# Kernel optimization log

Measured on AMD Instinct MI355X. Metric: run time of the kernel, lower is better.

Reference implementation:

```python
import jax, jax.numpy as jnp
import numpy as np

N_NODES = 20000
N_EDGES = 200000
C = 64             # channel multiplicity (hidden_irreps = 64x0e + 64x1o)
LMAX = 3
NLM = (LMAX + 1) ** 2   # 16 spherical-harmonic components
NUM_ELEM = 10
R_DIM = 8          # radial embedding out dim
MLP_H = 64
AVG_NEI = 10.0
L_OF_LM = np.repeat(np.arange(LMAX + 1), 2 * np.arange(LMAX + 1) + 1)  # [16] l index per lm slot


def setup_inputs() -> dict:
    key = jax.random.key(0)
    k = jax.random.split(key, 16)
    f32 = jnp.float32
    elems = jax.random.randint(k[0], (N_NODES,), 0, NUM_ELEM)
    one_hot = jax.nn.one_hot(elems, NUM_ELEM, dtype=f32)
    node_features = jax.random.normal(k[1], (N_NODES, C), dtype=f32)
    angular_embedding = jax.random.normal(k[2], (N_EDGES, NLM), dtype=f32)
    radial_embedding = jax.random.normal(k[3], (N_EDGES, R_DIM), dtype=f32)
    edge_index = jax.random.randint(k[4], (2, N_EDGES), 0, N_NODES)

    def w(kk, shape, fan_in):  # e3nn-style 1/sqrt(fan_in) normalization baked into init
        return jax.random.normal(kk, shape, dtype=f32) / float(np.sqrt(fan_in))

    W_up = w(k[5], (C, C), C)
    W_mlp1 = w(k[6], (R_DIM, MLP_H), R_DIM)
    W_mlp2 = w(k[7], (MLP_H, MLP_H), MLP_H)
    W_mlp3 = w(k[8], (MLP_H, MLP_H), MLP_H)
    W_mlp4 = w(k[9], (MLP_H, (LMAX + 1) * C), MLP_H)
    W_lin = w(k[10], (LMAX + 1, C, C), C)
    W_skip = w(k[11], (C, NUM_ELEM, C), C * NUM_ELEM)
    W_c0 = jax.random.normal(k[12], (NUM_ELEM, C), dtype=f32)
    W_c1 = jax.random.normal(k[13], (NUM_ELEM, C), dtype=f32)
    W_p0 = w(k[14], (C, C), C)
    W_p1 = w(k[15], (C, C), C)
    return dict(node_features=node_features, one_hot=one_hot,
                angular_embedding=angular_embedding, radial_embedding=radial_embedding,
                W_up=W_up, W_mlp1=W_mlp1, W_mlp2=W_mlp2, W_mlp3=W_mlp3, W_mlp4=W_mlp4,
                W_lin=W_lin, W_skip=W_skip, W_c0=W_c0, W_c1=W_c1, W_p0=W_p0, W_p1=W_p1,
                edge_index=edge_index)


def reference(node_features, one_hot, angular_embedding, radial_embedding,
              W_up, W_mlp1, W_mlp2, W_mlp3, W_mlp4, W_lin, W_skip,
              W_c0, W_c1, W_p0, W_p1, edge_index):
    sender, receiver = edge_index[0], edge_index[1]
    n = node_features.shape[0]
    # ---- interaction block (RealAgnosticResidual; node feats are pure scalars 64x0e) ----
    x = node_features @ W_up                                    # linear_up [N,C]
    h = jax.nn.silu(radial_embedding @ W_mlp1)                  # radial MLP -> per-edge TP weights
    h = jax.nn.silu(h @ W_mlp2)
    h = jax.nn.silu(h @ W_mlp3)
    tp_w = (h @ W_mlp4).reshape(-1, LMAX + 1, C)                # [E,4,C] (one weight per l path, uvu)
    w_lm = tp_w[:, L_OF_LM, :]                                  # [E,16,C]
    # uvu tensor product of 0e node feats with spherical harmonics (CG trivial for 0e x l -> l)
    msg = x[sender][:, None, :] * angular_embedding[:, :, None] * w_lm   # [E,16,C]
    agg = jax.ops.segment_sum(msg, receiver, num_segments=n) / AVG_NEI   # scatter-sum [N,16,C]
    feats = jnp.einsum('nmc,mck->nmk', agg, W_lin[L_OF_LM])     # per-l channel-mixing linear [N,16,C]
    # residual skip FCTP(64x0e, 10x0e -> hidden): only the 0e block is connected
    sc0 = jnp.einsum('nc,na,cak->nk', node_features, one_hot, W_skip)    # [N,C]
    # ---- equivariant product basis block (correlation = 1) ----
    wn0 = one_hot @ W_c0                                        # element-dependent weights [N,C]
    wn1 = one_hot @ W_c1
    f0 = feats[:, 0, :] * wn0                                   # l=0 output [N,C]
    f1 = feats[:, 1:4, :] * wn1[:, None, :]                     # l=1 output [N,3,C]
    out0 = f0 @ W_p0 + sc0                                      # [N,C]
    out1 = jnp.einsum('nmc,ck->nmk', f1, W_p1)                  # [N,3,C] (sc 1o block is zero)
    # flatten to e3nn channel-major irreps layout -> node_env [N, C*(1+3)]
    return jnp.concatenate([out0, jnp.swapaxes(out1, 1, 2).reshape(n, -1)], axis=-1)
```

## Files before the change

### kernel.cpp

```cpp
#include <hip/hip_runtime.h>

typedef __attribute__((ext_vector_type(8))) short s16x8;
typedef __attribute__((ext_vector_type(4))) float f32x4;

__device__ inline float bf2f(ushort u) {
    union { unsigned int i; float f; } v; v.i = ((unsigned)u) << 16; return v.f;
}
__device__ inline float u2f(unsigned u) {
    union { unsigned int i; float f; } v; v.i = u; return v.f;
}
__device__ inline ushort f2bf(float f) {
    union { float f; unsigned int i; } v; v.f = f;
    unsigned r = v.i + 0x7FFFu + ((v.i >> 16) & 1u);
    return (ushort)(r >> 16);
}
__device__ inline unsigned cvt_pk(float lo, float hi) {
    unsigned d;
    asm("v_cvt_pk_bf16_f32 %0, %1, %2" : "=v"(d) : "v"(lo), "v"(hi));
    return d;
}
__device__ inline float silu_f(float x) {
    float e;
    asm("v_exp_f32 %0, %1" : "=v"(e) : "v"(x * -1.44269504f));
    float d = 1.f + e, r;
    asm("v_rcp_f32 %0, %1" : "=v"(r) : "v"(d));
    return x * r;
}

__global__ __launch_bounds__(256) void prep_up_kernel(
    const float* __restrict__ nf, const float* __restrict__ W_up,
    ushort* __restrict__ x_ws,
    const float* __restrict__ W1, const float* __restrict__ W2,
    const float* __restrict__ W3, const float* __restrict__ W4,
    const float* __restrict__ W_lin, const float* __restrict__ Wp0,
    const float* __restrict__ Wp1, const float* __restrict__ W_skip,
    ushort* __restrict__ wimg, int* __restrict__ counts, int N) {
    __shared__ float sW[64 * 64];
    __shared__ float sNf[32][64];
    int tid = threadIdx.x;
    int nub = N / 32;
    if ((int)blockIdx.x < nub) {
        size_t n0 = (size_t)blockIdx.x * 32;
        for (int i = tid; i < 4096; i += 256) sW[i] = W_up[i];
        for (int i = tid; i < 2048; i += 256) {
            int r = i >> 6, c = i & 63;
            sNf[r][c] = nf[(n0 + r) * 64 + c];
        }
        __syncthreads();
        int r = tid >> 3, k0 = (tid & 7) * 8;
        float acc[8] = {0, 0, 0, 0, 0, 0, 0, 0};
        #pragma unroll 4
        for (int c = 0; c < 64; ++c) {
            float v = sNf[r][c];
            const float* wr = &sW[c * 64 + k0];
            #pragma unroll
            for (int j = 0; j < 8; ++j) acc[j] += v * wr[j];
        }
        uint4 val;
        val.x = cvt_pk(acc[0], acc[1]);
        val.y = cvt_pk(acc[2], acc[3]);
        val.z = cvt_pk(acc[4], acc[5]);
        val.w = cvt_pk(acc[6], acc[7]);
        *(uint4*)(x_ws + (n0 + r) * 64 + k0) = val;
        return;
    }
    int idx = ((int)blockIdx.x - nub) * 256 + tid;
    if (idx < N) counts[idx] = 0;
    if (idx < 4096) {
        int m = idx >> 6, k = idx & 63;
        int dst = m * 64 + ((((k >> 3) ^ (m & 7))) << 3) + (k & 7);
        wimg[dst] = (k < 8) ? f2bf(W1[k * 64 + m]) : (ushort)0;
    } else if (idx < 8192) {
        int i = idx - 4096;
        int m = i >> 6, k = i & 63;
        int dst = 4096 + m * 64 + ((((k >> 3) ^ (m & 7))) << 3) + (k & 7);
        wimg[dst] = f2bf(W2[k * 64 + m]);
    } else if (idx < 12288) {
        int i = idx - 8192;
        int m = i >> 6, k = i & 63;
        int dst = 8192 + m * 64 + ((((k >> 3) ^ (m & 7))) << 3) + (k & 7);
        wimg[dst] = f2bf(W3[k * 64 + m]);
    } else if (idx < 20480) {
        int i = idx - 12288;
        int m = i >> 6, k = i & 63;
        int dst = 12288 + m * 64 + ((((k >> 3) ^ (m & 7))) << 3) + (k & 7);
        wimg[dst] = f2bf(W4[k * 256 + m]);
    } else if (idx < 29696) {
        int i = idx - 20480;
        int row = i / 72, k = i % 72;
        int l = row >> 6, col = row & 63;
        wimg[idx] = (k < 64) ? f2bf(W_lin[l * 4096 + k * 64 + col]) : (ushort)0;
    } else if (idx < 38912) {
        int i = idx - 29696;
        int row = i / 72, k = i % 72;
        int l = row >> 6, col = row & 63;
        const float* Wp = l ? Wp1 : Wp0;
        wimg[idx] = (k < 64) ? f2bf(Wp[k * 64 + col]) : (ushort)0;
    } else if (idx < 79872) {
        int i = idx - 38912;
        wimg[idx] = f2bf(W_skip[i]);
    }
}

__global__ __launch_bounds__(256) void hist_kernel(const int* __restrict__ recv,
                                                   int* __restrict__ counts,
                                                   int* __restrict__ rank, int E) {
    int e = blockIdx.x * 256 + threadIdx.x;
    if (e < E) rank[e] = atomicAdd(&counts[recv[e]], 1);
}

__global__ __launch_bounds__(1024) void scan_kernel(const int* __restrict__ counts,
                                                    int* __restrict__ offsets, int n) {
    __shared__ int wsums[16];
    int tid = threadIdx.x, lane = tid & 63, wid = tid >> 6;
    int CH = (n + 1023) >> 10;
    int base = tid * CH;
    int cnt[20];
    int tot = 0;
    if (CH <= 20) {
        #pragma unroll
        for (int j = 0; j < 20; ++j) {
            int i = base + j;
            cnt[j] = (j < CH && i < n) ? counts[i] : 0;
            tot += cnt[j];
        }
    } else {
        for (int j = 0; j < CH; ++j) {
            int i = base + j;
            if (i < n) tot += counts[i];
        }
    }
    int v = tot;
    for (int off = 1; off < 64; off <<= 1) {
        int t = __shfl_up(v, off, 64);
        if (lane >= off) v += t;
    }
    if (lane == 63) wsums[wid] = v;
    __syncthreads();
    if (tid == 0) {
        int acc = 0;
        for (int w = 0; w < 16; ++w) { int t = wsums[w]; wsums[w] = acc; acc += t; }
    }
    __syncthreads();
    int excl = wsums[wid] + v - tot;
    if (CH <= 20) {
        #pragma unroll
        for (int j = 0; j < 20; ++j) {
            int i = base + j;
            if (j < CH && i < n) { offsets[i] = excl; excl += cnt[j]; }
        }
    } else {
        for (int j = 0; j < CH; ++j) {
            int i = base + j;
            if (i < n) { offsets[i] = excl; excl += counts[i]; }
        }
    }
    if (tid == 1023) offsets[n] = excl;
}

__global__ __launch_bounds__(256) void edge_mlp_kernel(
    const int* __restrict__ recv, const int* __restrict__ sender,
    const int* __restrict__ rank, const int* __restrict__ offsets,
    const float* __restrict__ radial, int2* __restrict__ csr_es,
    const ushort* __restrict__ wimg, unsigned* __restrict__ tpw32, int E) {
    __shared__ __align__(16) ushort sB[4][2048];
    int tid = threadIdx.x, lane = tid & 63, wave = tid >> 6;
    int n = lane & 15, hi = lane >> 4;
    int base = blockIdx.x * 128 + wave * 32;
    if (base >= E) return;
    int eA = base + n, eB = base + 16 + n;
    bool okA = eA < E, okB = eB < E;
    int eAc = min(eA, E - 1), eBc = min(eB, E - 1);

    char* bAq = (char*)sB[wave];
    char* bBq = (char*)sB[wave] + 2048;
    int n7 = n & 7;

    s16x8 bRA, bRB;
    #pragma unroll
    for (int j = 0; j < 8; ++j) { bRA[j] = 0; bRB[j] = 0; }
    if (hi == 0) {
        float4 a0 = *(const float4*)(radial + (size_t)eAc * 8);
        float4 a1 = *(const float4*)(radial + (size_t)eAc * 8 + 4);
        float4 c0 = *(const float4*)(radial + (size_t)eBc * 8);
        float4 c1 = *(const float4*)(radial + (size_t)eBc * 8 + 4);
        union { s16x8 v; uint4 u; } pa, pb;
        pa.u.x = cvt_pk(a0.x, a0.y); pa.u.y = cvt_pk(a0.z, a0.w);
        pa.u.z = cvt_pk(a1.x, a1.y); pa.u.w = cvt_pk(a1.z, a1.w);
        pb.u.x = cvt_pk(c0.x, c0.y); pb.u.y = cvt_pk(c0.z, c0.w);
        pb.u.z = cvt_pk(c1.x, c1.y); pb.u.w = cvt_pk(c1.z, c1.w);
        bRA = pa.v; bRB = pb.v;
        if (okA) {
            int2 es; es.x = eA; es.y = sender[eA];
            csr_es[offsets[recv[eA]] + rank[eA]] = es;
        }
        if (okB) {
            int2 es; es.x = eB; es.y = sender[eB];
            csr_es[offsets[recv[eB]] + rank[eB]] = es;
        }
    }

    f32x4 zero = {0.f, 0.f, 0.f, 0.f};
    f32x4 dA[4], dB[4];

    #pragma unroll
    for (int mt = 0; mt < 4; ++mt) {
        int row = mt * 16 + n, r7 = row & 7;
        s16x8 w = *(const s16x8*)(wimg + row * 64 + ((hi ^ r7) << 3));
        dA[mt] = __builtin_amdgcn_mfma_f32_16x16x32_bf16(w, bRA, zero, 0, 0, 0);
        dB[mt] = __builtin_amdgcn_mfma_f32_16x16x32_bf16(w, bRB, zero, 0, 0, 0);
    }
    #pragma unroll
    for (int mt = 0; mt < 4; ++mt) {
        int slot = mt * 2 + (hi >> 1);
        int off = ((slot ^ n7) << 4) + (hi & 1) * 8;
        uint2 vA = {cvt_pk(silu_f(dA[mt][0]), silu_f(dA[mt][1])),
                    cvt_pk(silu_f(dA[mt][2]), silu_f(dA[mt][3]))};
        *(uint2*)(bAq + n * 128 + off) = vA;
        uint2 vB = {cvt_pk(silu_f(dB[mt][0]), silu_f(dB[mt][1])),
                    cvt_pk(silu_f(dB[mt][2]), silu_f(dB[mt][3]))};
        *(uint2*)(bBq + n * 128 + off) = vB;
    }
    s16x8 b0A = *(const s16x8*)(bAq + n * 128 + ((hi ^ n7) << 4));
    s16x8 b1A = *(const s16x8*)(bAq + n * 128 + (((4 + hi) ^ n7) << 4));
    s16x8 b0B = *(const s16x8*)(bBq + n * 128 + ((hi ^ n7) << 4));
    s16x8 b1B = *(const s16x8*)(bBq + n * 128 + (((4 + hi) ^ n7) << 4));

    #pragma unroll
    for (int mt = 0; mt < 4; ++mt) {
        int row = mt * 16 + n, r7 = row & 7;
        s16x8 w0 = *(const s16x8*)(wimg + 4096 + row * 64 + ((hi ^ r7) << 3));
        s16x8 w1 = *(const s16x8*)(wimg + 4096 + row * 64 + (((4 + hi) ^ r7) << 3));
        dA[mt] = __builtin_amdgcn_mfma_f32_16x16x32_bf16(w0, b0A, zero, 0, 0, 0);
        dA[mt] = __builtin_amdgcn_mfma_f32_16x16x32_bf16(w1, b1A, dA[mt], 0, 0, 0);
        dB[mt] = __builtin_amdgcn_mfma_f32_16x16x32_bf16(w0, b0B, zero, 0, 0, 0);
        dB[mt] = __builtin_amdgcn_mfma_f32_16x16x32_bf16(w1, b1B, dB[mt], 0, 0, 0);
    }
    #pragma unroll
    for (int mt = 0; mt < 4; ++mt) {
        int slot = mt * 2 + (hi >> 1);
        int off = ((slot ^ n7) << 4) + (hi & 1) * 8;
        uint2 vA = {cvt_pk(silu_f(dA[mt][0]), silu_f(dA[mt][1])),
                    cvt_pk(silu_f(dA[mt][2]), silu_f(dA[mt][3]))};
        *(uint2*)(bAq + n * 128 + off) = vA;
        uint2 vB = {cvt_pk(silu_f(dB[mt][0]), silu_f(dB[mt][1])),
                    cvt_pk(silu_f(dB[mt][2]), silu_f(dB[mt][3]))};
        *(uint2*)(bBq + n * 128 + off) = vB;
    }
    b0A = *(const s16x8*)(bAq + n * 128 + ((hi ^ n7) << 4));
    b1A = *(const s16x8*)(bAq + n * 128 + (((4 + hi) ^ n7) << 4));
    b0B = *(const s16x8*)(bBq + n * 128 + ((hi ^ n7) << 4));
    b1B = *(const s16x8*)(bBq + n * 128 + (((4 + hi) ^ n7) << 4));

    #pragma unroll
    for (int mt = 0; mt < 4; ++mt) {
        int row = mt * 16 + n, r7 = row & 7;
        s16x8 w0 = *(const s16x8*)(wimg + 8192 + row * 64 + ((hi ^ r7) << 3));
        s16x8 w1 = *(const s16x8*)(wimg + 8192 + row * 64 + (((4 + hi) ^ r7) << 3));
        dA[mt] = __builtin_amdgcn_mfma_f32_16x16x32_bf16(w0, b0A, zero, 0, 0, 0);
        dA[mt] = __builtin_amdgcn_mfma_f32_16x16x32_bf16(w1, b1A, dA[mt], 0, 0, 0);
        dB[mt] = __builtin_amdgcn_mfma_f32_16x16x32_bf16(w0, b0B, zero, 0, 0, 0);
        dB[mt] = __builtin_amdgcn_mfma_f32_16x16x32_bf16(w1, b1B, dB[mt], 0, 0, 0);
    }
    #pragma unroll
    for (int mt = 0; mt < 4; ++mt) {
        int slot = mt * 2 + (hi >> 1);
        int off = ((slot ^ n7) << 4) + (hi & 1) * 8;
        uint2 vA = {cvt_pk(silu_f(dA[mt][0]), silu_f(dA[mt][1])),
                    cvt_pk(silu_f(dA[mt][2]), silu_f(dA[mt][3]))};
        *(uint2*)(bAq + n * 128 + off) = vA;
        uint2 vB = {cvt_pk(silu_f(dB[mt][0]), silu_f(dB[mt][1])),
                    cvt_pk(silu_f(dB[mt][2]), silu_f(dB[mt][3]))};
        *(uint2*)(bBq + n * 128 + off) = vB;
    }
    b0A = *(const s16x8*)(bAq + n * 128 + ((hi ^ n7) << 4));
    b1A = *(const s16x8*)(bAq + n * 128 + (((4 + hi) ^ n7) << 4));
    b0B = *(const s16x8*)(bBq + n * 128 + ((hi ^ n7) << 4));
    b1B = *(const s16x8*)(bBq + n * 128 + (((4 + hi) ^ n7) << 4));

    size_t rbA = (size_t)eA * 64, rbB = (size_t)eB * 64;
    const ushort* w4 = wimg + 12288;
    #pragma unroll
    for (int mt = 0; mt < 4; ++mt) {
        int row0 = mt * 16 + n, r70 = row0 & 7;
        int row1 = (mt + 4) * 16 + n, r71 = row1 & 7;
        s16x8 a0lo = *(const s16x8*)(w4 + row0 * 64 + ((hi ^ r70) << 3));
        s16x8 a1lo = *(const s16x8*)(w4 + row0 * 64 + (((4 + hi) ^ r70) << 3));
        s16x8 a0hi = *(const s16x8*)(w4 + row1 * 64 + ((hi ^ r71) << 3));
        s16x8 a1hi = *(const s16x8*)(w4 + row1 * 64 + (((4 + hi) ^ r71) << 3));
        f32x4 oloA = __builtin_amdgcn_mfma_f32_16x16x32_bf16(a0lo, b0A, zero, 0, 0, 0);
        oloA = __builtin_amdgcn_mfma_f32_16x16x32_bf16(a1lo, b1A, oloA, 0, 0, 0);
        f32x4 ohiA = __builtin_amdgcn_mfma_f32_16x16x32_bf16(a0hi, b0A, zero, 0, 0, 0);
        ohiA = __builtin_amdgcn_mfma_f32_16x16x32_bf16(a1hi, b1A, ohiA, 0, 0, 0);
        f32x4 oloB = __builtin_amdgcn_mfma_f32_16x16x32_bf16(a0lo, b0B, zero, 0, 0, 0);
        oloB = __builtin_amdgcn_mfma_f32_16x16x32_bf16(a1lo, b1B, oloB, 0, 0, 0);
        f32x4 ohiB = __builtin_amdgcn_mfma_f32_16x16x32_bf16(a0hi, b0B, zero, 0, 0, 0);
        ohiB = __builtin_amdgcn_mfma_f32_16x16x32_bf16(a1hi, b1B, ohiB, 0, 0, 0);
        if (okA) {
            uint4 val;
            val.x = cvt_pk(oloA[0], ohiA[0]);
            val.y = cvt_pk(oloA[1], ohiA[1]);
            val.z = cvt_pk(oloA[2], ohiA[2]);
            val.w = cvt_pk(oloA[3], ohiA[3]);
            *(uint4*)(tpw32 + rbA + mt * 16 + hi * 4) = val;
        }
        if (okB) {
            uint4 val;
            val.x = cvt_pk(oloB[0], ohiB[0]);
            val.y = cvt_pk(oloB[1], ohiB[1]);
            val.z = cvt_pk(oloB[2], ohiB[2]);
            val.w = cvt_pk(oloB[3], ohiB[3]);
            *(uint4*)(tpw32 + rbB + mt * 16 + hi * 4) = val;
        }
    }
}

__global__ __launch_bounds__(256) void agg_kernel(const float* __restrict__ angular,
                                                  const int2* __restrict__ csr_es,
                                                  const unsigned* __restrict__ tpw32,
                                                  const int* __restrict__ offsets,
                                                  const ushort* __restrict__ x_ws,
                                                  ushort* __restrict__ agg, int N) {
    int wave = threadIdx.x >> 6, lane = threadIdx.x & 63;
    int node = blockIdx.x * 4 + wave;
    if (node >= N) return;
    int beg = offsets[node], end = offsets[node + 1];
    float a0 = 0, a1 = 0, a2 = 0, a3 = 0;
    for (int cb = beg; cb < end; cb += 64) {
        int m = min(64, end - cb);
        int2 es = csr_es[cb + min(lane, m - 1)];
        int ev = es.x, sv = es.y;
        for (int e0 = 0; e0 < m; e0 += 8) {
            unsigned t[8];
            ushort x[8];
            float4 g[8];
            #pragma unroll
            for (int j = 0; j < 8; ++j) {
                int e = e0 + j;
                int ec = min(e, m - 1);
                int eidj = __shfl(ev, ec);
                t[j] = tpw32[(size_t)eidj * 64 + lane];
                x[j] = x_ws[(size_t)__shfl(sv, ec) * 64 + lane];
                if (e < m) g[j] = *(const float4*)(angular + (size_t)eidj * 16);
                else g[j] = make_float4(0.f, 0.f, 0.f, 0.f);
            }
            #pragma unroll
            for (int j = 0; j < 8; ++j) {
                float xv = bf2f(x[j]);
                float tp0 = u2f(t[j] << 16);
                float tp1 = u2f(t[j] & 0xffff0000u);
                float y0 = xv * tp0, y1 = xv * tp1;
                a0 += g[j].x * y0;
                a1 += g[j].y * y1;
                a2 += g[j].z * y1;
                a3 += g[j].w * y1;
            }
        }
    }
    size_t b = (size_t)node * 256 + lane;
    agg[b] = f2bf(a0 * 0.1f);
    agg[b + 64] = f2bf(a1 * 0.1f);
    agg[b + 128] = f2bf(a2 * 0.1f);
    agg[b + 192] = f2bf(a3 * 0.1f);
}

__global__ __launch_bounds__(256) void node_out2_kernel(
    const float* __restrict__ nf, const float* __restrict__ one_hot,
    const ushort* __restrict__ wimg, const float* __restrict__ W_c0,
    const float* __restrict__ W_c1, const ushort* __restrict__ agg,
    float* __restrict__ out) {
    __shared__ __align__(16) ushort sWl[2 * 64 * 72];
    __shared__ __align__(16) ushort sF[4][32 * 72];
    __shared__ float sSc[32][64];
    __shared__ float sWc[2][640];
    __shared__ int sElem[32];
    int tid = threadIdx.x;
    int n0 = blockIdx.x * 32;
    int lane = tid & 63, m = tid >> 6;
    int lsel = (m == 0) ? 0 : 1;

    s16x8 pf[4][2];
    #pragma unroll
    for (int nt = 0; nt < 4; ++nt)
        #pragma unroll
        for (int ks = 0; ks < 2; ++ks)
            pf[nt][ks] = *(const s16x8*)(wimg + 29696 +
                (lsel * 64 + nt * 16 + (lane & 15)) * 72 + ks * 32 + (lane >> 4) * 8);

    for (int i = tid; i < 1152; i += 256)
        ((s16x8*)sWl)[i] = ((const s16x8*)(wimg + 20480))[i];
    for (int i = tid; i < 1280; i += 256)
        sWc[i >= 640][i % 640] = (i >= 640 ? W_c1 : W_c0)[i % 640];
    if (tid < 32) {
        int nn = n0 + tid, e = 0;
        for (int a = 0; a < 10; ++a)
            if (one_hot[(size_t)nn * 10 + a] > 0.5f) { e = a; break; }
        sElem[tid] = e;
    }
    __syncthreads();

    {
        int nl = tid >> 3, k0 = (tid & 7) * 8;
        int nn = n0 + nl, elem = sElem[nl];
        float acc[8] = {0, 0, 0, 0, 0, 0, 0, 0};
        const ushort* wskb = wimg + 38912;
        for (int c = 0; c < 64; ++c) {
            float v = nf[(size_t)nn * 64 + c];
            s16x8 w = *(const s16x8*)(wskb + ((size_t)c * 10 + elem) * 64 + k0);
            #pragma unroll
            for (int j = 0; j < 8; ++j) acc[j] += v * bf2f((ushort)w[j]);
        }
        #pragma unroll
        for (int j = 0; j < 8; ++j) sSc[nl][k0 + j] = acc[j];
    }

    f32x4 acc[2][4] = {};
    s16x8 afr[2][2];
    #pragma unroll
    for (int mt = 0; mt < 2; ++mt)
        #pragma unroll
        for (int ks = 0; ks < 2; ++ks)
            afr[mt][ks] = *(const s16x8*)(agg +
                (((size_t)(n0 + mt * 16 + (lane & 15))) * 4 + m) * 64 +
                ks * 32 + (lane >> 4) * 8);
    #pragma unroll
    for (int nt = 0; nt < 4; ++nt)
        #pragma unroll
        for (int ks = 0; ks < 2; ++ks) {
            s16x8 b = *(const s16x8*)(sWl + (lsel * 64 + nt * 16 + (lane & 15)) * 72 +
                                      ks * 32 + (lane >> 4) * 8);
            #pragma unroll
            for (int mt = 0; mt < 2; ++mt)
                acc[mt][nt] = __builtin_amdgcn_mfma_f32_16x16x32_bf16(afr[mt][ks], b,
                                                                      acc[mt][nt], 0, 0, 0);
        }

    #pragma unroll
    for (int mt = 0; mt < 2; ++mt)
        #pragma unroll
        for (int nt = 0; nt < 4; ++nt)
            #pragma unroll
            for (int r = 0; r < 4; ++r) {
                int nl = mt * 16 + (lane >> 4) * 4 + r;
                int k = nt * 16 + (lane & 15);
                float scale = sWc[lsel][sElem[nl] * 64 + k];
                sF[m][nl * 72 + k] = f2bf(acc[mt][nt][r] * scale);
            }
    __syncthreads();

    f32x4 acc2[2][4] = {};
    s16x8 af2[2][2];
    #pragma unroll
    for (int mt = 0; mt < 2; ++mt)
        #pragma unroll
        for (int ks = 0; ks < 2; ++ks)
            af2[mt][ks] = *(const s16x8*)(&sF[m][(mt * 16 + (lane & 15)) * 72 +
                                                 ks * 32 + (lane >> 4) * 8]);
    #pragma unroll
    for (int nt = 0; nt < 4; ++nt)
        #pragma unroll
        for (int ks = 0; ks < 2; ++ks) {
            #pragma unroll
            for (int mt = 0; mt < 2; ++mt)
                acc2[mt][nt] = __builtin_amdgcn_mfma_f32_16x16x32_bf16(af2[mt][ks],
                                                                       pf[nt][ks],
                                                                       acc2[mt][nt], 0, 0, 0);
        }

    #pragma unroll
    for (int mt = 0; mt < 2; ++mt)
        #pragma unroll
        for (int nt = 0; nt < 4; ++nt)
            #pragma unroll
            for (int r = 0; r < 4; ++r) {
                int nl = mt * 16 + (lane >> 4) * 4 + r;
                int k = nt * 16 + (lane & 15);
                size_t nn = (size_t)n0 + nl;
                if (m == 0)
                    out[nn * 256 + k] = acc2[mt][nt][r] + sSc[nl][k];
                else
                    out[nn * 256 + 64 + k * 3 + (m - 1)] = acc2[mt][nt][r];
            }
}

extern "C" void kernel_launch(void* const* d_in, const int* in_sizes, int n_in,
                              void* d_out, int out_size, void* d_ws, size_t ws_size,
                              hipStream_t stream) {
    const float* node_features = (const float*)d_in[0];
    const float* one_hot = (const float*)d_in[1];
    const float* angular = (const float*)d_in[2];
    const float* radial = (const float*)d_in[3];
    const float* W_up = (const float*)d_in[4];
    const float* W_mlp1 = (const float*)d_in[5];
    const float* W_mlp2 = (const float*)d_in[6];
    const float* W_mlp3 = (const float*)d_in[7];
    const float* W_mlp4 = (const float*)d_in[8];
    const float* W_lin = (const float*)d_in[9];
    const float* W_skip = (const float*)d_in[10];
    const float* W_c0 = (const float*)d_in[11];
    const float* W_c1 = (const float*)d_in[12];
    const float* W_p0 = (const float*)d_in[13];
    const float* W_p1 = (const float*)d_in[14];
    const int* edge_index = (const int*)d_in[15];
    float* out = (float*)d_out;

    int N = in_sizes[0] / 64;
    int E = in_sizes[2] / 16;
    const int* sender = edge_index;
    const int* receiver = edge_index + E;

    char* p = (char*)d_ws;
    ushort* x_ws = (ushort*)p;      p += (size_t)N * 64 * 2;
    unsigned* tpw32 = (unsigned*)p; p += (size_t)E * 64 * 4;
    ushort* agg = (ushort*)p;       p += (size_t)N * 256 * 2;
    ushort* wimg = (ushort*)p;      p += 79872 * 2;
    int* counts = (int*)p;          p += (size_t)N * 4;
    int* offsets = (int*)p;         p += (size_t)(N + 1) * 4;
    int* rank = (int*)p;            p += (size_t)E * 4;
    int2* csr_es = (int2*)p;        p += (size_t)E * 8;

    prep_up_kernel<<<N / 32 + 312, 256, 0, stream>>>(node_features, W_up, x_ws,
                                                     W_mlp1, W_mlp2, W_mlp3, W_mlp4,
                                                     W_lin, W_p0, W_p1, W_skip, wimg,
                                                     counts, N);
    hist_kernel<<<(E + 255) / 256, 256, 0, stream>>>(receiver, counts, rank, E);
    scan_kernel<<<1, 1024, 0, stream>>>(counts, offsets, N);
    edge_mlp_kernel<<<(E + 127) / 128, 256, 0, stream>>>(receiver, sender, rank,
                                                         offsets, radial, csr_es,
                                                         wimg, tpw32, E);
    agg_kernel<<<(N + 3) / 4, 256, 0, stream>>>(angular, csr_es, tpw32,
                                                offsets, x_ws, agg, N);
    node_out2_kernel<<<N / 32, 256, 0, stream>>>(node_features, one_hot, wimg,
                                                 W_c0, W_c1, agg, out);
}
```

Baseline: 107.6 us.

## Fuse edge aggregation into node output kernel via shared-memory agg tile

Result: slower. 115.9 us (+7.7%).

```diff
diff --git a/kernel.cpp b/kernel.cpp
--- a/kernel.cpp
+++ b/kernel.cpp
@@ -315,81 +315,25 @@
     }
 }
 
-__global__ __launch_bounds__(256) void agg_kernel(const float* __restrict__ angular,
-                                                  const int2* __restrict__ csr_es,
-                                                  const unsigned* __restrict__ tpw32,
-                                                  const int* __restrict__ offsets,
-                                                  const ushort* __restrict__ x_ws,
-                                                  ushort* __restrict__ agg, int N) {
-    int wave = threadIdx.x >> 6, lane = threadIdx.x & 63;
-    int node = blockIdx.x * 4 + wave;
-    if (node >= N) return;
-    int beg = offsets[node], end = offsets[node + 1];
-    float a0 = 0, a1 = 0, a2 = 0, a3 = 0;
-    for (int cb = beg; cb < end; cb += 64) {
-        int m = min(64, end - cb);
-        int2 es = csr_es[cb + min(lane, m - 1)];
-        int ev = es.x, sv = es.y;
-        for (int e0 = 0; e0 < m; e0 += 8) {
-            unsigned t[8];
-            ushort x[8];
-            float4 g[8];
-            #pragma unroll
-            for (int j = 0; j < 8; ++j) {
-                int e = e0 + j;
-                int ec = min(e, m - 1);
-                int eidj = __shfl(ev, ec);
-                t[j] = tpw32[(size_t)eidj * 64 + lane];
-                x[j] = x_ws[(size_t)__shfl(sv, ec) * 64 + lane];
-                if (e < m) g[j] = *(const float4*)(angular + (size_t)eidj * 16);
-                else g[j] = make_float4(0.f, 0.f, 0.f, 0.f);
-            }
-            #pragma unroll
-            for (int j = 0; j < 8; ++j) {
-                float xv = bf2f(x[j]);
-                float tp0 = u2f(t[j] << 16);
-                float tp1 = u2f(t[j] & 0xffff0000u);
-                float y0 = xv * tp0, y1 = xv * tp1;
-                a0 += g[j].x * y0;
-                a1 += g[j].y * y1;
-                a2 += g[j].z * y1;
-                a3 += g[j].w * y1;
-            }
-        }
-    }
-    size_t b = (size_t)node * 256 + lane;
-    agg[b] = f2bf(a0 * 0.1f);
-    agg[b + 64] = f2bf(a1 * 0.1f);
-    agg[b + 128] = f2bf(a2 * 0.1f);
-    agg[b + 192] = f2bf(a3 * 0.1f);
-}
-
-__global__ __launch_bounds__(256) void node_out2_kernel(
-    const float* __restrict__ nf, const float* __restrict__ one_hot,
-    const ushort* __restrict__ wimg, const float* __restrict__ W_c0,
-    const float* __restrict__ W_c1, const ushort* __restrict__ agg,
-    float* __restrict__ out) {
+__global__ __launch_bounds__(512) void agg_out_kernel(
+    const float* __restrict__ angular, const int2* __restrict__ csr_es,
+    const unsigned* __restrict__ tpw32, const int* __restrict__ offsets,
+    const ushort* __restrict__ x_ws, const float* __restrict__ nf,
+    const float* __restrict__ one_hot, const ushort* __restrict__ wimg,
+    const float* __restrict__ W_c0, const float* __restrict__ W_c1,
+    float* __restrict__ out, int N) {
+    __shared__ __align__(16) ushort sAgg[32 * 264];
     __shared__ __align__(16) ushort sWl[2 * 64 * 72];
     __shared__ __align__(16) ushort sF[4][32 * 72];
     __shared__ float sSc[32][64];
     __shared__ float sWc[2][640];
     __shared__ int sElem[32];
-    int tid = threadIdx.x;
+    int tid = threadIdx.x, lane = tid & 63, wv = tid >> 6;
     int n0 = blockIdx.x * 32;
-    int lane = tid & 63, m = tid >> 6;
-    int lsel = (m == 0) ? 0 : 1;
-
-    s16x8 pf[4][2];
-    #pragma unroll
-    for (int nt = 0; nt < 4; ++nt)
-        #pragma unroll
-        for (int ks = 0; ks < 2; ++ks)
-            pf[nt][ks] = *(const s16x8*)(wimg + 29696 +
-                (lsel * 64 + nt * 16 + (lane & 15)) * 72 + ks * 32 + (lane >> 4) * 8);
-
-    for (int i = tid; i < 1152; i += 256)
+
+    for (int i = tid; i < 1152; i += 512)
         ((s16x8*)sWl)[i] = ((const s16x8*)(wimg + 20480))[i];
-    for (int i = tid; i < 1280; i += 256)
+    for (int i = tid; i < 1280; i += 512)
         sWc[i >= 640][i % 640] = (i >= 640 ? W_c1 : W_c0)[i % 640];
     if (tid < 32) {
         int nn = n0 + tid, e = 0;
@@ -397,90 +341,146 @@
             if (one_hot[(size_t)nn * 10 + a] > 0.5f) { e = a; break; }
         sElem[tid] = e;
     }
+
+    int m = wv;
+    int lsel = (m == 0) ? 0 : 1;
+    s16x8 pf[4][2];
+    if (wv < 4) {
+        #pragma unroll
+        for (int nt = 0; nt < 4; ++nt)
+            #pragma unroll
+            for (int ks = 0; ks < 2; ++ks)
+                pf[nt][ks] = *(const s16x8*)(wimg + 29696 +
+                    (lsel * 64 + nt * 16 + (lane & 15)) * 72 + ks * 32 +
+                    (lane >> 4) * 8);
+    }
+
+    for (int q = 0; q < 4; ++q) {
+        int node = n0 + wv * 4 + q;
+        int beg = offsets[node], end = offsets[node + 1];
+        float a0 = 0, a1 = 0, a2 = 0, a3 = 0;
+        for (int cb = beg; cb < end; cb += 64) {
+            int mm = min(64, end - cb);
+            int2 es = csr_es[cb + min(lane, mm - 1)];
+            int ev = es.x, sv = es.y;
+            for (int e0 = 0; e0 < mm; e0 += 8) {
+                unsigned t[8];
+                ushort x[8];
+                float4 g[8];
+                #pragma unroll
+                for (int j = 0; j < 8; ++j) {
+                    int e = e0 + j;
+                    int ec = min(e, mm - 1);
+                    int eidj = __shfl(ev, ec);
+                    t[j] = tpw32[(size_t)eidj * 64 + lane];
+                    x[j] = x_ws[(size_t)__shfl(sv, ec) * 64 + lane];
+                    if (e < mm) g[j] = *(const float4*)(angular + (size_t)eidj * 16);
+                    else g[j] = make_float4(0.f, 0.f, 0.f, 0.f);
+                }
+                #pragma unroll
+                for (int j = 0; j < 8; ++j) {
+                    float xv = bf2f(x[j]);
+                    float tp0 = u2f(t[j] << 16);
+                    float tp1 = u2f(t[j] & 0xffff0000u);
+                    float y0 = xv * tp0, y1 = xv * tp1;
+                    a0 += g[j].x * y0;
+                    a1 += g[j].y * y1;
+                    a2 += g[j].z * y1;
+                    a3 += g[j].w * y1;
+                }
+            }
+        }
+        int row = wv * 4 + q;
+        sAgg[row * 264 + lane] = f2bf(a0 * 0.1f);
+        sAgg[row * 264 + 64 + lane] = f2bf(a1 * 0.1f);
+        sAgg[row * 264 + 128 + lane] = f2bf(a2 * 0.1f);
+        sAgg[row * 264 + 192 + lane] = f2bf(a3 * 0.1f);
+    }
     __syncthreads();
 
-    {
-        int nl = tid >> 3, k0 = (tid & 7) * 8;
+    if (wv >= 4) {
+        int t2 = tid - 256;
+        int nl = t2 >> 3, k0 = (t2 & 7) * 8;
         int nn = n0 + nl, elem = sElem[nl];
-        float acc[8] = {0, 0, 0, 0, 0, 0, 0, 0};
+        float acc8[8] = {0, 0, 0, 0, 0, 0, 0, 0};
         const ushort* wskb = wimg + 38912;
         for (int c = 0; c < 64; ++c) {
             float v = nf[(size_t)nn * 64 + c];
             s16x8 w = *(const s16x8*)(wskb + ((size_t)c * 10 + elem) * 64 + k0);
             #pragma unroll
-            for (int j = 0; j < 8; ++j) acc[j] += v * bf2f((ushort)w[j]);
-        }
-        #pragma unroll
-        for (int j = 0; j < 8; ++j) sSc[nl][k0 + j] = acc[j];
-    }
-
-    f32x4 acc[2][4] = {};
-    s16x8 afr[2][2];
-    #pragma unroll
-    for (int mt = 0; mt < 2; ++mt)
-        #pragma unroll
-        for (int ks = 0; ks < 2; ++ks)
-            afr[mt][ks] = *(const s16x8*)(agg +
-                (((size_t)(n0 + mt * 16 + (lane & 15))) * 4 + m) * 64 +
-                ks * 32 + (lane >> 4) * 8);
-    #pragma unroll
-    for (int nt = 0; nt < 4; ++nt)
-        #pragma unroll
-        for (int ks = 0; ks < 2; ++ks) {
-            s16x8 b = *(const s16x8*)(sWl + (lsel * 64 + nt * 16 + (lane & 15)) * 72 +
-                                      ks * 32 + (lane >> 4) * 8);
-            #pragma unroll
-            for (int mt = 0; mt < 2; ++mt)
-                acc[mt][nt] = __builtin_amdgcn_mfma_f32_16x16x32_bf16(afr[mt][ks], b,
-                                                                      acc[mt][nt], 0, 0, 0);
-        }
-
-    #pragma unroll
-    for (int mt = 0; mt < 2; ++mt)
+            for (int j = 0; j < 8; ++j) acc8[j] += v * bf2f((ushort)w[j]);
+        }
+        #pragma unroll
+        for (int j = 0; j < 8; ++j) sSc[nl][k0 + j] = acc8[j];
+    } else {
+        f32x4 acc[2][4] = {};
+        s16x8 afr[2][2];
+        #pragma unroll
+        for (int mt = 0; mt < 2; ++mt)
+            #pragma unroll
+            for (int ks = 0; ks < 2; ++ks)
+                afr[mt][ks] = *(const s16x8*)(sAgg +
+                    (mt * 16 + (lane & 15)) * 264 + m * 64 + ks * 32 +
+                    (lane >> 4) * 8);
         #pragma unroll
         for (int nt = 0; nt < 4; ++nt)
             #pragma unroll
-            for (int r = 0; r < 4; ++r) {
-                int nl = mt * 16 + (lane >> 4) * 4 + r;
-                int k = nt * 16 + (lane & 15);
-                float scale = sWc[lsel][sElem[nl] * 64 + k];
-                sF[m][nl * 72 + k] = f2bf(acc[mt][nt][r] * scale);
+            for (int ks = 0; ks < 2; ++ks) {
+                s16x8 b = *(const s16x8*)(sWl +
+                    (lsel * 64 + nt * 16 + (lane & 15)) * 72 + ks * 32 +
+                    (lane >> 4) * 8);
+                #pragma unroll
+                for (int mt = 0; mt < 2; ++mt)
+                    acc[mt][nt] = __builtin_amdgcn_mfma_f32_16x16x32_bf16(
+                        afr[mt][ks], b, acc[mt][nt], 0, 0, 0);
             }
+        #pragma unroll
+        for (int mt = 0; mt < 2; ++mt)
+            #pragma unroll
+            for (int nt = 0; nt < 4; ++nt)
+                #pragma unroll
+                for (int r = 0; r < 4; ++r) {
+                    int nl = mt * 16 + (lane >> 4) * 4 + r;
+                    int k = nt * 16 + (lane & 15);
+                    float scale = sWc[lsel][sElem[nl] * 64 + k];
+                    sF[m][nl * 72 + k] = f2bf(acc[mt][nt][r] * scale);
+                }
+    }
     __syncthreads();
 
-    f32x4 acc2[2][4] = {};
-    s16x8 af2[2][2];
-    #pragma unroll
-    for (int mt = 0; mt < 2; ++mt)
-        #pragma unroll
-        for (int ks = 0; ks < 2; ++ks)
-            af2[mt][ks] = *(const s16x8*)(&sF[m][(mt * 16 + (lane & 15)) * 72 +
-                                                 ks * 32 + (lane >> 4) * 8]);
-    #pragma unroll
-    for (int nt = 0; nt < 4; ++nt)
-        #pragma unroll
-        for (int ks = 0; ks < 2; ++ks) {
-            #pragma unroll
-            for (int mt = 0; mt < 2; ++mt)
-                acc2[mt][nt] = __builtin_amdgcn_mfma_f32_16x16x32_bf16(af2[mt][ks],
-                                                                       pf[nt][ks],
-                                                                       acc2[mt][nt], 0, 0, 0);
-        }
-
-    #pragma unroll
-    for (int mt = 0; mt < 2; ++mt)
+    if (wv < 4) {
+        f32x4 acc2[2][4] = {};
+        s16x8 af2[2][2];
+        #pragma unroll
+        for (int mt = 0; mt < 2; ++mt)
+            #pragma unroll
+            for (int ks = 0; ks < 2; ++ks)
+                af2[mt][ks] = *(const s16x8*)(&sF[m][(mt * 16 + (lane & 15)) * 72 +
+                                                     ks * 32 + (lane >> 4) * 8]);
         #pragma unroll
         for (int nt = 0; nt < 4; ++nt)
             #pragma unroll
-            for (int r = 0; r < 4; ++r) {
-                int nl = mt * 16 + (lane >> 4) * 4 + r;
-                int k = nt * 16 + (lane & 15);
-                size_t nn = (size_t)n0 + nl;
-                if (m == 0)
-                    out[nn * 256 + k] = acc2[mt][nt][r] + sSc[nl][k];
-                else
-                    out[nn * 256 + 64 + k * 3 + (m - 1)] = acc2[mt][nt][r];
+            for (int ks = 0; ks < 2; ++ks) {
+                #pragma unroll
+                for (int mt = 0; mt < 2; ++mt)
+                    acc2[mt][nt] = __builtin_amdgcn_mfma_f32_16x16x32_bf16(
+                        af2[mt][ks], pf[nt][ks], acc2[mt][nt], 0, 0, 0);
             }
+        #pragma unroll
+        for (int mt = 0; mt < 2; ++mt)
+            #pragma unroll
+            for (int nt = 0; nt < 4; ++nt)
+                #pragma unroll
+                for (int r = 0; r < 4; ++r) {
+                    int nl = mt * 16 + (lane >> 4) * 4 + r;
+                    int k = nt * 16 + (lane & 15);
+                    size_t nn = (size_t)n0 + nl;
+                    if (m == 0)
+                        out[nn * 256 + k] = acc2[mt][nt][r] + sSc[nl][k];
+                    else
+                        out[nn * 256 + 64 + k * 3 + (m - 1)] = acc2[mt][nt][r];
+                }
+    }
 }
 
 extern "C" void kernel_launch(void* const* d_in, const int* in_sizes, int n_in,
@@ -512,7 +512,6 @@
     char* p = (char*)d_ws;
     ushort* x_ws = (ushort*)p;      p += (size_t)N * 64 * 2;
     unsigned* tpw32 = (unsigned*)p; p += (size_t)E * 64 * 4;
-    ushort* agg = (ushort*)p;       p += (size_t)N * 256 * 2;
     ushort* wimg = (ushort*)p;      p += 79872 * 2;
     int* counts = (int*)p;          p += (size_t)N * 4;
     int* offsets = (int*)p;         p += (size_t)(N + 1) * 4;
@@ -528,8 +527,7 @@
     edge_mlp_kernel<<<(E + 127) / 128, 256, 0, stream>>>(receiver, sender, rank,
                                                          offsets, radial, csr_es,
                                                          wimg, tpw32, E);
-    agg_kernel<<<(N + 3) / 4, 256, 0, stream>>>(angular, csr_es, tpw32,
-                                                offsets, x_ws, agg, N);
-    node_out2_kernel<<<N / 32, 256, 0, stream>>>(node_features, one_hot, wimg,
-                                                 W_c0, W_c1, agg, out);
-}
+    agg_out_kernel<<<N / 32, 512, 0, stream>>>(angular, csr_es, tpw32, offsets,
+                                               x_ws, node_features, one_hot, wimg,
+                                               W_c0, W_c1, out, N);
+}
```
